# Kernel optimization log

Measured on AMD Instinct MI355X. Metric: run time of the kernel, lower is better.

The kernel has to match this reference:

```python
import jax, jax.numpy as jnp
import numpy as np

E1 = 150000   # number of 1-hop edges
E2 = 150000   # number of 2-hop edges
T = 400000    # triangles per triangle class
C = 64        # in_channels
H = 64        # mlp_hidden_channels
L = 2         # num DR2FWL2Conv layers
N_MLP = 8     # MLPs per conv layer


def setup_inputs() -> dict:
    key = jax.random.key(0)
    ks = jax.random.split(key, 20)
    edge_attr = jax.random.normal(ks[0], (E1, C), jnp.float32)
    edge_attr2 = jax.random.normal(ks[1], (E2, C), jnp.float32)
    # triangle index tensors: rows (ij, ik, kj); hop type of each row decides the range
    triangle_1_1_1 = jax.random.randint(ks[2], (3, T), 0, E1)
    triangle_1_1_2 = jnp.stack([jax.random.randint(jax.random.fold_in(ks[3], r), (T,), 0, m)
                                for r, m in enumerate([E1, E1, E2])])
    triangle_1_2_2 = jnp.stack([jax.random.randint(jax.random.fold_in(ks[4], r), (T,), 0, m)
                                for r, m in enumerate([E1, E2, E2])])
    triangle_2_2_2 = jax.random.randint(ks[5], (3, T), 0, E2)
    inverse_edge_1 = jax.random.permutation(ks[6], E1)
    inverse_edge_2 = jax.random.permutation(ks[7], E2)
    s = 0.05
    mlp_w1 = jax.random.normal(ks[8], (L, N_MLP, C, H), jnp.float32) * s
    mlp_b1 = jnp.zeros((L, N_MLP, H), jnp.float32)
    mlp_w2 = jax.random.normal(ks[9], (L, N_MLP, H, C), jnp.float32) * s
    mlp_b2 = jnp.zeros((L, N_MLP, C), jnp.float32)
    lin_w1 = jax.random.normal(ks[10], (C, C), jnp.float32) * s
    lin_b1 = jnp.zeros((C,), jnp.float32)
    lin_w2 = jax.random.normal(ks[11], (C, C), jnp.float32) * s
    lin_b2 = jnp.zeros((C,), jnp.float32)
    return dict(edge_attr=edge_attr, edge_attr2=edge_attr2,
                triangle_1_1_1=triangle_1_1_1, triangle_1_1_2=triangle_1_1_2,
                triangle_1_2_2=triangle_1_2_2, triangle_2_2_2=triangle_2_2_2,
                inverse_edge_1=inverse_edge_1, inverse_edge_2=inverse_edge_2,
                mlp_w1=mlp_w1, mlp_b1=mlp_b1, mlp_w2=mlp_w2, mlp_b2=mlp_b2,
                lin_w1=lin_w1, lin_b1=lin_b1, lin_w2=lin_w2, lin_b2=lin_b2)


def reference(edge_attr, edge_attr2, triangle_1_1_1, triangle_1_1_2,
              triangle_1_2_2, triangle_2_2_2, inverse_edge_1, inverse_edge_2,
              mlp_w1, mlp_b1, mlp_w2, mlp_b2, lin_w1, lin_b1, lin_w2, lin_b2):
    eps = 0.0
    eps2 = 0.0
    ij111, ik111, kj111 = triangle_1_1_1
    ij112, ik112, kj112 = triangle_1_1_2
    ij122, ik122, kj122 = triangle_1_2_2
    ij222, ik222, kj222 = triangle_2_2_2
    seg = jax.ops.segment_sum

    e1, e2 = edge_attr, edge_attr2
    n1, n2 = e1.shape[0], e2.shape[0]
    for li in range(mlp_w1.shape[0]):
        def mlp(x, mi, li=li):
            h = jax.nn.relu(x @ mlp_w1[li, mi] + mlp_b1[li, mi])
            return h @ mlp_w2[li, mi] + mlp_b2[li, mi]
        m111 = seg(mlp(e1[ik111], 0) * mlp(e1[kj111], 0), ij111, num_segments=n1)
        m112 = seg(mlp(e1[ik112], 1) * mlp(e2[kj112], 2), ij112, num_segments=n1)
        m122 = seg(mlp(e2[ik122], 3) * mlp(e2[kj122], 3), ij122, num_segments=n1)
        e1 = e1 * (1.0 + eps) + m111 + m112 + m112[inverse_edge_1] + m122
        m211 = seg(mlp(e1[ij112], 4) * mlp(e1[ik112], 4), kj112, num_segments=n2)
        m212 = seg(mlp(e1[ij122], 5) * mlp(e2[kj122], 6), ik122, num_segments=n2)
        m222 = seg(mlp(e2[ik222], 7) * mlp(e2[kj222], 7), ij222, num_segments=n2)
        e2 = e2 * (1.0 + eps2) + m211 + m212 + m212[inverse_edge_2] + m222
        # norm=None (Identity), relu after, dropout=0 in eval
        e1, e2 = jax.nn.relu(e1), jax.nn.relu(e2)
    return (e1 @ lin_w1 + lin_b1, e2 @ lin_w2 + lin_b2)
```

## Files before the change

kernel.cpp:

```cpp
#include <hip/hip_runtime.h>
#include <hip/hip_fp16.h>


typedef unsigned short u16;
typedef unsigned int u32;
typedef _Float16 f16;
typedef __attribute__((ext_vector_type(8))) short s16x8;
typedef __attribute__((ext_vector_type(4))) float f32x4;
typedef __attribute__((ext_vector_type(4))) _Float16 f16x4;

#define MFMA16(a, b, c) __builtin_amdgcn_mfma_f32_16x16x32_bf16((a), (b), (c), 0, 0, 0)

static __device__ __forceinline__ u16 bf16_rne(float x) {
  u32 u = __float_as_uint(x);
  return (u16)((u + 0x7fffu + ((u >> 16) & 1u)) >> 16);
}
static __device__ __forceinline__ float bf16_f32(u16 h) {
  return __uint_as_float(((u32)h) << 16);
}
static __device__ __forceinline__ void cvt_hilo8(const f32x4 a, const f32x4 b, s16x8& hi, s16x8& lo) {
#pragma unroll
  for (int j = 0; j < 4; j++) {
    float x = a[j];
    u16 h = bf16_rne(x);
    u16 l = bf16_rne(x - bf16_f32(h));
    hi[j] = (short)h; lo[j] = (short)l;
  }
#pragma unroll
  for (int j = 0; j < 4; j++) {
    float x = b[j];
    u16 h = bf16_rne(x);
    u16 l = bf16_rne(x - bf16_f32(h));
    hi[4 + j] = (short)h; lo[4 + j] = (short)l;
  }
}

__global__ __launch_bounds__(256) void repack_split_kernel(const float* __restrict__ src,
                                                           u16* __restrict__ hi, u16* __restrict__ lo, int nmat) {
  int o = blockIdx.x * 256 + threadIdx.x;
  int stride = gridDim.x * 256;
  int total = nmat * 4096;
  for (; o < total; o += stride) {
    int m = o >> 12, r = o & 4095;
    int j = r & 7, lane = (r >> 3) & 63, nt = (r >> 9) & 3, kt = (r >> 11) & 1;
    int k = kt * 32 + ((lane >> 4) << 3) + j;
    int n = nt * 16 + (lane & 15);
    float x = src[(size_t)m * 4096 + k * 64 + n];
    u16 h = bf16_rne(x);
    hi[o] = h;
    lo[o] = bf16_rne(x - bf16_f32(h));
  }
}

__global__ __launch_bounds__(256) void copy_kernel(const float* __restrict__ src, float* __restrict__ dst, int n4) {
  int i = blockIdx.x * 256 + threadIdx.x;
  int stride = gridDim.x * 256;
  const f32x4* s4 = (const f32x4*)src;
  f32x4* d4 = (f32x4*)dst;
  for (; i < n4; i += stride) d4[i] = s4[i];
}

__global__ __launch_bounds__(256) void relu_kernel(float* __restrict__ e, int n4) {
  int i = blockIdx.x * 256 + threadIdx.x;
  int stride = gridDim.x * 256;
  f32x4* e4 = (f32x4*)e;
  for (; i < n4; i += stride) {
    f32x4 v = e4[i];
#pragma unroll
    for (int j = 0; j < 4; j++) v[j] = fmaxf(v[j], 0.0f);
    e4[i] = v;
  }
}

template <bool DO_RELU>
__global__ __launch_bounds__(256) void addinv2_kernel(float* __restrict__ e, const f16* __restrict__ A,
                                                      const f16* __restrict__ B, const int* __restrict__ inv, int E) {
  int i = blockIdx.x * 256 + threadIdx.x;
  int stride = gridDim.x * 256;
  int total = E * 16;
  f32x4* e4 = (f32x4*)e;
  const f16x4* A4 = (const f16x4*)A;
  const f16x4* B4 = (const f16x4*)B;
  for (; i < total; i += stride) {
    int r = i >> 4, q = i & 15;
    int ir = inv[r];
    f32x4 v = e4[i];
    f16x4 a = A4[i];
    f16x4 b = B4[i];
    f16x4 bi = B4[(size_t)ir * 16 + q];
#pragma unroll
    for (int j = 0; j < 4; j++) {
      float x = v[j] + (float)a[j] + (float)b[j] + (float)bi[j];
      v[j] = DO_RELU ? fmaxf(x, 0.0f) : x;
    }
    e4[i] = v;
  }
}

__global__ __launch_bounds__(256) void seg3_kernel(
    __half2* __restrict__ dstA, __half2* __restrict__ dstB,
    const __half2* __restrict__ paA, const __half2* __restrict__ pbA,
    const int* __restrict__ iA0, const int* __restrict__ iA1, const int* __restrict__ iA2,
    const __half2* __restrict__ paB, const __half2* __restrict__ pbB,
    const int* __restrict__ iB0, const int* __restrict__ iB1, const int* __restrict__ iB2,
    const __half2* __restrict__ paC, const __half2* __restrict__ pbC,
    const int* __restrict__ iC0, const int* __restrict__ iC1, const int* __restrict__ iC2,
    int T) {
  int i = blockIdx.x * 256 + threadIdx.x;
  int stride = gridDim.x * 256;
  int total = 3 * T * 32;
  for (; i < total; i += stride) {
    int u = i >> 5, cp = i & 31;
    __half2* dst;
    const __half2 *pa, *pb;
    const int *i0, *i1, *i2;
    int t;
    if (u < T) { t = u; dst = dstA; pa = paA; pb = pbA; i0 = iA0; i1 = iA1; i2 = iA2; }
    else if (u < 2 * T) { t = u - T; dst = dstB; pa = paB; pb = pbB; i0 = iB0; i1 = iB1; i2 = iB2; }
    else { t = u - 2 * T; dst = dstA; pa = paC; pb = pbC; i0 = iC0; i1 = iC1; i2 = iC2; }
    __half2 va = pa[(size_t)i1[t] * 32 + cp];
    __half2 vb = pb[(size_t)i2[t] * 32 + cp];
    float2 fa = __half22float2(va), fb = __half22float2(vb);
    __half2 prod = __floats2half2_rn(fa.x * fb.x, fa.y * fb.y);
    unsafeAtomicAdd(&dst[(size_t)i0[t] * 32 + cp], prod);
  }
}

__global__ __launch_bounds__(256) void mlp4_kernel(
    const float* __restrict__ srcA, const float* __restrict__ srcB,
    f16* __restrict__ d0, f16* __restrict__ d1, f16* __restrict__ d2, f16* __restrict__ d3,
    const u16* __restrict__ w1h_, const u16* __restrict__ w1l_,
    const u16* __restrict__ w2h_, const u16* __restrict__ w2l_,
    const float* __restrict__ b1_, const float* __restrict__ b2_, int s1, int s2) {
  __shared__ float hshm[4][1024];
  const int tid = threadIdx.x;
  const int wave = tid >> 6, lane = tid & 63;
  const int lrow = lane & 15, lk = lane >> 4;
  const int gw = (blockIdx.x * 256 + tid) >> 6;
  const int total = 2 * s1 + 2 * s2;
  if (gw >= total) return;

  int mi, strip;
  const float* src;
  f16* dst;
  if (gw < s1) { mi = 0; strip = gw; src = srcA; dst = d0; }
  else if (gw < 2 * s1) { mi = 1; strip = gw - s1; src = srcA; dst = d1; }
  else if (gw < 2 * s1 + s2) { mi = 2; strip = gw - 2 * s1; src = srcB; dst = d2; }
  else { mi = 3; strip = gw - 2 * s1 - s2; src = srcB; dst = d3; }

  const s16x8* W1H = (const s16x8*)(w1h_ + (size_t)mi * 4096);
  const s16x8* W1L = (const s16x8*)(w1l_ + (size_t)mi * 4096);
  const s16x8* W2H = (const s16x8*)(w2h_ + (size_t)mi * 4096);
  const s16x8* W2L = (const s16x8*)(w2l_ + (size_t)mi * 4096);
  s16x8 w1h[2][4], w1l[2][4], w2h[2][4], w2l[2][4];
#pragma unroll
  for (int kt = 0; kt < 2; kt++)
#pragma unroll
    for (int nt = 0; nt < 4; nt++) {
      const int f = (kt * 4 + nt) * 64 + lane;
      w1h[kt][nt] = W1H[f];
      w1l[kt][nt] = W1L[f];
      w2h[kt][nt] = W2H[f];
      w2l[kt][nt] = W2L[f];
    }
  float bias1[4], bias2[4];
#pragma unroll
  for (int nt = 0; nt < 4; nt++) {
    bias1[nt] = b1_[mi * 64 + nt * 16 + lrow];
    bias2[nt] = b2_[mi * 64 + nt * 16 + lrow];
  }

  float* hl = hshm[wave];
  const float* xp = src + (size_t)(strip * 16 + lrow) * 64 + lk * 8;
  f32x4 x0 = *(const f32x4*)(xp + 0);
  f32x4 x1 = *(const f32x4*)(xp + 4);
  f32x4 x2 = *(const f32x4*)(xp + 32);
  f32x4 x3 = *(const f32x4*)(xp + 36);
  s16x8 ah[2], al[2];
  cvt_hilo8(x0, x1, ah[0], al[0]);
  cvt_hilo8(x2, x3, ah[1], al[1]);

  f32x4 acc[4];
#pragma unroll
  for (int nt = 0; nt < 4; nt++) { acc[nt][0] = bias1[nt]; acc[nt][1] = bias1[nt]; acc[nt][2] = bias1[nt]; acc[nt][3] = bias1[nt]; }
#pragma unroll
  for (int kt = 0; kt < 2; kt++)
#pragma unroll
    for (int nt = 0; nt < 4; nt++) {
      acc[nt] = MFMA16(ah[kt], w1h[kt][nt], acc[nt]);
      acc[nt] = MFMA16(ah[kt], w1l[kt][nt], acc[nt]);
      acc[nt] = MFMA16(al[kt], w1h[kt][nt], acc[nt]);
    }

#pragma unroll
  for (int nt = 0; nt < 4; nt++)
#pragma unroll
    for (int r = 0; r < 4; r++) {
      const int row = lk * 4 + r;
      const int col = nt * 16 + lrow;
      hl[row * 64 + (col ^ ((row & 7) << 2))] = fmaxf(acc[nt][r], 0.0f);
    }
  s16x8 bh[2], bl[2];
#pragma unroll
  for (int kt = 0; kt < 2; kt++) {
    const int colb = kt * 32 + lk * 8;
    const int xr = (lrow & 7) << 2;
    f32x4 h0 = *(const f32x4*)&hl[lrow * 64 + ((colb + 0) ^ xr)];
    f32x4 h1 = *(const f32x4*)&hl[lrow * 64 + ((colb + 4) ^ xr)];
    cvt_hilo8(h0, h1, bh[kt], bl[kt]);
  }

  f32x4 out[4];
#pragma unroll
  for (int nt = 0; nt < 4; nt++) { out[nt][0] = bias2[nt]; out[nt][1] = bias2[nt]; out[nt][2] = bias2[nt]; out[nt][3] = bias2[nt]; }
#pragma unroll
  for (int kt = 0; kt < 2; kt++)
#pragma unroll
    for (int nt = 0; nt < 4; nt++) {
      out[nt] = MFMA16(bh[kt], w2h[kt][nt], out[nt]);
      out[nt] = MFMA16(bh[kt], w2l[kt][nt], out[nt]);
      out[nt] = MFMA16(bl[kt], w2h[kt][nt], out[nt]);
    }

  f16* dp = dst + (size_t)strip * 1024;
#pragma unroll
  for (int nt = 0; nt < 4; nt++)
#pragma unroll
    for (int r = 0; r < 4; r++)
      dp[(lk * 4 + r) * 64 + nt * 16 + lrow] = (f16)out[nt][r];
}

__global__ __launch_bounds__(256) void lin_kernel(const float* __restrict__ src, float* __restrict__ dst,
                                                  const u16* __restrict__ wh_, const u16* __restrict__ wl_,
                                                  const float* __restrict__ b_, int nstrips) {
  const int tid = threadIdx.x;
  const int wave = tid >> 6, lane = tid & 63;
  const int lrow = lane & 15, lk = lane >> 4;

  const s16x8* WH = (const s16x8*)wh_;
  const s16x8* WL = (const s16x8*)wl_;
  s16x8 wh[2][4], wl[2][4];
#pragma unroll
  for (int kt = 0; kt < 2; kt++)
#pragma unroll
    for (int nt = 0; nt < 4; nt++) {
      const int f = (kt * 4 + nt) * 64 + lane;
      wh[kt][nt] = WH[f];
      wl[kt][nt] = WL[f];
    }
  float bias[4];
#pragma unroll
  for (int nt = 0; nt < 4; nt++) bias[nt] = b_[nt * 16 + lrow];

  for (int s = blockIdx.x * 4 + wave; s < nstrips; s += gridDim.x * 4) {
    const float* xp = src + (size_t)(s * 16 + lrow) * 64 + lk * 8;
    f32x4 x0 = *(const f32x4*)(xp + 0);
    f32x4 x1 = *(const f32x4*)(xp + 4);
    f32x4 x2 = *(const f32x4*)(xp + 32);
    f32x4 x3 = *(const f32x4*)(xp + 36);
    s16x8 ah[2], al[2];
    cvt_hilo8(x0, x1, ah[0], al[0]);
    cvt_hilo8(x2, x3, ah[1], al[1]);

    f32x4 acc[4];
#pragma unroll
    for (int nt = 0; nt < 4; nt++) { acc[nt][0] = bias[nt]; acc[nt][1] = bias[nt]; acc[nt][2] = bias[nt]; acc[nt][3] = bias[nt]; }
#pragma unroll
    for (int kt = 0; kt < 2; kt++)
#pragma unroll
      for (int nt = 0; nt < 4; nt++) {
        acc[nt] = MFMA16(ah[kt], wh[kt][nt], acc[nt]);
        acc[nt] = MFMA16(ah[kt], wl[kt][nt], acc[nt]);
        acc[nt] = MFMA16(al[kt], wh[kt][nt], acc[nt]);
      }
    float* dp = dst + (size_t)s * 1024;
#pragma unroll
    for (int nt = 0; nt < 4; nt++)
#pragma unroll
      for (int r = 0; r < 4; r++)
        dp[(lk * 4 + r) * 64 + nt * 16 + lrow] = acc[nt][r];
  }
}

extern "C" void kernel_launch(void* const* d_in, const int* in_sizes, int n_in,
                              void* d_out, int out_size, void* d_ws, size_t ws_size,
                              hipStream_t stream) {
  const float* in_e1 = (const float*)d_in[0];
  const float* in_e2 = (const float*)d_in[1];
  const int* t111 = (const int*)d_in[2];
  const int* t112 = (const int*)d_in[3];
  const int* t122 = (const int*)d_in[4];
  const int* t222 = (const int*)d_in[5];
  const int* inv1 = (const int*)d_in[6];
  const int* inv2 = (const int*)d_in[7];
  const float* mw1 = (const float*)d_in[8];
  const float* mb1 = (const float*)d_in[9];
  const float* mw2 = (const float*)d_in[10];
  const float* mb2 = (const float*)d_in[11];
  const float* lw1 = (const float*)d_in[12];
  const float* lb1 = (const float*)d_in[13];
  const float* lw2 = (const float*)d_in[14];
  const float* lb2 = (const float*)d_in[15];

  const int E1 = in_sizes[0] / 64, E2 = in_sizes[1] / 64;
  const int T = in_sizes[2] / 3;
  const int L = in_sizes[8] / (8 * 64 * 64);
  const size_t nE1 = (size_t)E1 * 64, nE2 = (size_t)E2 * 64;
  const size_t nMax = nE1 > nE2 ? nE1 : nE2;

  float* e1b = (float*)d_ws;
  float* e2b = e1b + nE1;
  f16* mA = (f16*)(e2b + nE2);
  f16* mB = mA + nMax;
  f16* p0 = mB + nMax;
  f16* p1 = p0 + nE1;
  const size_t wmat = (size_t)L * 8 * 4096;
  u16* w1h = (u16*)(p1 + nE1);
  u16* w1l = w1h + wmat;
  u16* w2h = w1l + wmat;
  u16* w2l = w2h + wmat;
  u16* lwh = w2l + wmat;
  u16* lwl = lwh + 8192;
  const size_t needB = (nE1 + nE2) * 4 + (2 * nMax + 2 * nE1) * 2 + (4 * wmat + 4 * 4096) * 2;
  if (ws_size < needB) return;

  f16* p2 = (f16*)d_out;
  f16* p3 = p2 + nE2;

  const int s1 = E1 / 16, s2 = E2 / 16;
  const int mlp4B = (2 * s1 + 2 * s2 + 3) / 4;
  const int SEGB = 2048, ELTB = 2048;

  repack_split_kernel<<<256, 256, 0, stream>>>(mw1, w1h, w1l, L * 8);
  repack_split_kernel<<<256, 256, 0, stream>>>(mw2, w2h, w2l, L * 8);
  repack_split_kernel<<<32, 256, 0, stream>>>(lw1, lwh, lwl, 1);
  repack_split_kernel<<<32, 256, 0, stream>>>(lw2, lwh + 4096, lwl + 4096, 1);

  copy_kernel<<<ELTB, 256, 0, stream>>>(in_e1, e1b, (int)(nE1 / 4));
  copy_kernel<<<ELTB, 256, 0, stream>>>(in_e2, e2b, (int)(nE2 / 4));

  for (int li = 0; li < L; li++) {
    const size_t mo = (size_t)li * 8 * 4096;
    const size_t bo = (size_t)li * 8 * 64;
    mlp4_kernel<<<mlp4B, 256, 0, stream>>>(e1b, e2b, p0, p1, p2, p3,
                                           w1h + mo, w1l + mo, w2h + mo, w2l + mo,
                                           mb1 + bo, mb2 + bo, s1, s2);
    hipMemsetAsync(mA, 0, 2 * nMax * 2, stream);
    seg3_kernel<<<SEGB, 256, 0, stream>>>(
        (__half2*)mA, (__half2*)mB,
        (const __half2*)p0, (const __half2*)p0, t111, t111 + T, t111 + 2 * T,
        (const __half2*)p1, (const __half2*)p2, t112, t112 + T, t112 + 2 * T,
        (const __half2*)p3, (const __half2*)p3, t122, t122 + T, t122 + 2 * T, T);
    addinv2_kernel<false><<<ELTB, 256, 0, stream>>>(e1b, mA, mB, inv1, E1);

    mlp4_kernel<<<mlp4B, 256, 0, stream>>>(e1b, e2b, p0, p1, p2, p3,
                                           w1h + mo + 4 * 4096, w1l + mo + 4 * 4096,
                                           w2h + mo + 4 * 4096, w2l + mo + 4 * 4096,
                                           mb1 + bo + 4 * 64, mb2 + bo + 4 * 64, s1, s2);
    hipMemsetAsync(mA, 0, 2 * nMax * 2, stream);
    seg3_kernel<<<SEGB, 256, 0, stream>>>(
        (__half2*)mA, (__half2*)mB,
        (const __half2*)p0, (const __half2*)p0, t112 + 2 * T, t112, t112 + T,
        (const __half2*)p1, (const __half2*)p2, t122 + T, t122, t122 + 2 * T,
        (const __half2*)p3, (const __half2*)p3, t222, t222 + T, t222 + 2 * T, T);
    addinv2_kernel<true><<<ELTB, 256, 0, stream>>>(e2b, mA, mB, inv2, E2);

    relu_kernel<<<ELTB, 256, 0, stream>>>(e1b, (int)(nE1 / 4));
  }

  lin_kernel<<<(s1 + 3) / 4, 256, 0, stream>>>(e1b, (float*)d_out, lwh, lwl, lb1, s1);
  lin_kernel<<<(s2 + 3) / 4, 256, 0, stream>>>(e2b, (float*)d_out + nE1, lwh + 4096, lwl + 4096, lb2, s2);
}
```

Before: 992.0 us.

## Replace atomic segment-sum scatter with CSR gather built once by counting sort

Builds per-class CSR row pointers and (A,B) index payloads once per call via histogram, three-pass scan, and scatter. Each segment-sum then becomes a gather kernel where one thread owns an output row/channel pair, accumulates in fp32 and adds straight into the edge features. This removes the fp16 atomic adds, the memsets and one accumulator buffer. The cost is a preprocessing pass with atomics on every call and uneven per-row loop lengths in the gather.

```diff
diff --git a/kernel.cpp b/kernel.cpp
--- a/kernel.cpp
+++ b/kernel.cpp
@@ -7,7 +7,6 @@
 typedef _Float16 f16;
 typedef __attribute__((ext_vector_type(8))) short s16x8;
 typedef __attribute__((ext_vector_type(4))) float f32x4;
-typedef __attribute__((ext_vector_type(4))) _Float16 f16x4;
 
 #define MFMA16(a, b, c) __builtin_amdgcn_mfma_f32_16x16x32_bf16((a), (b), (c), 0, 0, 0)
 
@@ -33,6 +32,140 @@
     u16 l = bf16_rne(x - bf16_f32(h));
     hi[4 + j] = (short)h; lo[4 + j] = (short)l;
   }
+}
+
+static __device__ __forceinline__ void class_ptrs(int c, const int* t111, const int* t112,
+                                                  const int* t122, const int* t222, int T,
+                                                  const int*& D, const int*& A, const int*& B) {
+  switch (c) {
+    case 0: D = t111;          A = t111 + T; B = t111 + 2 * T; break;
+    case 1: D = t112;          A = t112 + T; B = t112 + 2 * T; break;
+    case 2: D = t122;          A = t122 + T; B = t122 + 2 * T; break;
+    case 3: D = t112 + 2 * T;  A = t112;     B = t112 + T;     break;
+    case 4: D = t122 + T;      A = t122;     B = t122 + 2 * T; break;
+    default: D = t222;         A = t222 + T; B = t222 + 2 * T; break;
+  }
+}
+
+__global__ __launch_bounds__(256) void hist_kernel(int* __restrict__ pos,
+                                                   const int* t111, const int* t112,
+                                                   const int* t122, const int* t222, int T, int Emax) {
+  int i = blockIdx.x * 256 + threadIdx.x;
+  if (i >= 6 * T) return;
+  int c = i / T, t = i - c * T;
+  const int *D, *A, *B;
+  class_ptrs(c, t111, t112, t122, t222, T, D, A, B);
+  atomicAdd(&pos[(size_t)c * Emax + D[t]], 1);
+}
+
+__global__ __launch_bounds__(1024) void scanA_kernel(const int* __restrict__ pos, int* __restrict__ partial,
+                                                     int Emax, int E1, int E2, int NCH) {
+  __shared__ int sh[1024];
+  int c = blockIdx.x / NCH, ch = blockIdx.x % NCH;
+  int idx = ch * 1024 + threadIdx.x;
+  int Ec = c < 3 ? E1 : E2;
+  int v = (idx < Ec) ? pos[(size_t)c * Emax + idx] : 0;
+  sh[threadIdx.x] = v;
+  __syncthreads();
+  for (int s = 512; s > 0; s >>= 1) {
+    if (threadIdx.x < s) sh[threadIdx.x] += sh[threadIdx.x + s];
+    __syncthreads();
+  }
+  if (threadIdx.x == 0) partial[blockIdx.x] = sh[0];
+}
+
+__global__ __launch_bounds__(1024) void scanB_kernel(int* __restrict__ partial, int NCH) {
+  __shared__ int sh[1024];
+  for (int c = 0; c < 6; c++) {
+    int v = (threadIdx.x < NCH) ? partial[c * NCH + threadIdx.x] : 0;
+    sh[threadIdx.x] = v;
+    __syncthreads();
+    for (int off = 1; off < 1024; off <<= 1) {
+      int x = (threadIdx.x >= off) ? sh[threadIdx.x - off] : 0;
+      __syncthreads();
+      sh[threadIdx.x] += x;
+      __syncthreads();
+    }
+    if (threadIdx.x < NCH) partial[c * NCH + threadIdx.x] = sh[threadIdx.x] - v;
+    __syncthreads();
+  }
+}
+
+__global__ __launch_bounds__(1024) void scanC_kernel(int* __restrict__ pos, int* __restrict__ rp,
+                                                     const int* __restrict__ partial,
+                                                     int Emax, int E1, int E2, int NCH, int T) {
+  __shared__ int sh[1024];
+  int c = blockIdx.x / NCH, ch = blockIdx.x % NCH;
+  int idx = ch * 1024 + threadIdx.x;
+  int Ec = c < 3 ? E1 : E2;
+  int v = (idx < Ec) ? pos[(size_t)c * Emax + idx] : 0;
+  sh[threadIdx.x] = v;
+  __syncthreads();
+  for (int off = 1; off < 1024; off <<= 1) {
+    int x = (threadIdx.x >= off) ? sh[threadIdx.x - off] : 0;
+    __syncthreads();
+    sh[threadIdx.x] += x;
+    __syncthreads();
+  }
+  int excl = sh[threadIdx.x] - v;
+  int base = partial[blockIdx.x];
+  if (idx < Ec) {
+    int off = base + excl;
+    rp[(size_t)c * (Emax + 1) + idx] = off;
+    pos[(size_t)c * Emax + idx] = off;
+    if (idx == Ec - 1) rp[(size_t)c * (Emax + 1) + Ec] = off + v;
+  }
+}
+
+typedef struct { int x, y; } i2;
+
+__global__ __launch_bounds__(256) void scatter_kernel(int* __restrict__ pos, i2* __restrict__ payload,
+                                                      const int* t111, const int* t112,
+                                                      const int* t122, const int* t222, int T, int Emax) {
+  int i = blockIdx.x * 256 + threadIdx.x;
+  if (i >= 6 * T) return;
+  int c = i / T, t = i - c * T;
+  const int *D, *A, *B;
+  class_ptrs(c, t111, t112, t122, t222, T, D, A, B);
+  int slot = atomicAdd(&pos[(size_t)c * Emax + D[t]], 1);
+  i2 p; p.x = A[t]; p.y = B[t];
+  payload[(size_t)c * T + slot] = p;
+}
+
+__global__ __launch_bounds__(256) void segcsr_kernel(
+    float2* __restrict__ e, float2* __restrict__ mB,
+    const int* __restrict__ rpA, const i2* __restrict__ plA, const __half2* __restrict__ paA, const __half2* __restrict__ pbA,
+    const int* __restrict__ rpB, const i2* __restrict__ plB, const __half2* __restrict__ paB, const __half2* __restrict__ pbB,
+    const int* __restrict__ rpC, const i2* __restrict__ plC, const __half2* __restrict__ paC, const __half2* __restrict__ pbC,
+    int E) {
+  int i = blockIdx.x * 256 + threadIdx.x;
+  if (i >= E * 32) return;
+  int r = i >> 5, cp = i & 31;
+  float2 acc = e[(size_t)r * 32 + cp];
+  int b0 = rpA[r], b1 = rpA[r + 1];
+  for (int t = b0; t < b1; t++) {
+    i2 ab = plA[t];
+    float2 a = __half22float2(paA[(size_t)ab.x * 32 + cp]);
+    float2 b = __half22float2(pbA[(size_t)ab.y * 32 + cp]);
+    acc.x += a.x * b.x; acc.y += a.y * b.y;
+  }
+  b0 = rpC[r]; b1 = rpC[r + 1];
+  for (int t = b0; t < b1; t++) {
+    i2 ab = plC[t];
+    float2 a = __half22float2(paC[(size_t)ab.x * 32 + cp]);
+    float2 b = __half22float2(pbC[(size_t)ab.y * 32 + cp]);
+    acc.x += a.x * b.x; acc.y += a.y * b.y;
+  }
+  e[(size_t)r * 32 + cp] = acc;
+  float2 accB = make_float2(0.0f, 0.0f);
+  b0 = rpB[r]; b1 = rpB[r + 1];
+  for (int t = b0; t < b1; t++) {
+    i2 ab = plB[t];
+    float2 a = __half22float2(paB[(size_t)ab.x * 32 + cp]);
+    float2 b = __half22float2(pbB[(size_t)ab.y * 32 + cp]);
+    accB.x += a.x * b.x; accB.y += a.y * b.y;
+  }
+  mB[(size_t)r * 32 + cp] = accB;
 }
 
 __global__ __launch_bounds__(256) void repack_split_kernel(const float* __restrict__ src,
@@ -73,56 +206,25 @@
 }
 
 template <bool DO_RELU>
-__global__ __launch_bounds__(256) void addinv2_kernel(float* __restrict__ e, const f16* __restrict__ A,
-                                                      const f16* __restrict__ B, const int* __restrict__ inv, int E) {
+__global__ __launch_bounds__(256) void addinv_kernel(float* __restrict__ e, const float* __restrict__ B,
+                                                     const int* __restrict__ inv, int E) {
   int i = blockIdx.x * 256 + threadIdx.x;
   int stride = gridDim.x * 256;
   int total = E * 16;
   f32x4* e4 = (f32x4*)e;
-  const f16x4* A4 = (const f16x4*)A;
-  const f16x4* B4 = (const f16x4*)B;
+  const f32x4* B4 = (const f32x4*)B;
   for (; i < total; i += stride) {
     int r = i >> 4, q = i & 15;
     int ir = inv[r];
     f32x4 v = e4[i];
-    f16x4 a = A4[i];
-    f16x4 b = B4[i];
-    f16x4 bi = B4[(size_t)ir * 16 + q];
+    f32x4 b = B4[i];
+    f32x4 bi = B4[(size_t)ir * 16 + q];
 #pragma unroll
     for (int j = 0; j < 4; j++) {
-      float x = v[j] + (float)a[j] + (float)b[j] + (float)bi[j];
+      float x = v[j] + b[j] + bi[j];
       v[j] = DO_RELU ? fmaxf(x, 0.0f) : x;
     }
     e4[i] = v;
-  }
-}
-
-__global__ __launch_bounds__(256) void seg3_kernel(
-    __half2* __restrict__ dstA, __half2* __restrict__ dstB,
-    const __half2* __restrict__ paA, const __half2* __restrict__ pbA,
-    const int* __restrict__ iA0, const int* __restrict__ iA1, const int* __restrict__ iA2,
-    const __half2* __restrict__ paB, const __half2* __restrict__ pbB,
-    const int* __restrict__ iB0, const int* __restrict__ iB1, const int* __restrict__ iB2,
-    const __half2* __restrict__ paC, const __half2* __restrict__ pbC,
-    const int* __restrict__ iC0, const int* __restrict__ iC1, const int* __restrict__ iC2,
-    int T) {
-  int i = blockIdx.x * 256 + threadIdx.x;
-  int stride = gridDim.x * 256;
-  int total = 3 * T * 32;
-  for (; i < total; i += stride) {
-    int u = i >> 5, cp = i & 31;
-    __half2* dst;
-    const __half2 *pa, *pb;
-    const int *i0, *i1, *i2;
-    int t;
-    if (u < T) { t = u; dst = dstA; pa = paA; pb = pbA; i0 = iA0; i1 = iA1; i2 = iA2; }
-    else if (u < 2 * T) { t = u - T; dst = dstB; pa = paB; pb = pbB; i0 = iB0; i1 = iB1; i2 = iB2; }
-    else { t = u - 2 * T; dst = dstA; pa = paC; pb = pbC; i0 = iC0; i1 = iC1; i2 = iC2; }
-    __half2 va = pa[(size_t)i1[t] * 32 + cp];
-    __half2 vb = pb[(size_t)i2[t] * 32 + cp];
-    float2 fa = __half22float2(va), fb = __half22float2(vb);
-    __half2 prod = __floats2half2_rn(fa.x * fb.x, fa.y * fb.y);
-    unsafeAtomicAdd(&dst[(size_t)i0[t] * 32 + cp], prod);
   }
 }
 
@@ -305,14 +407,16 @@
   const int E1 = in_sizes[0] / 64, E2 = in_sizes[1] / 64;
   const int T = in_sizes[2] / 3;
   const int L = in_sizes[8] / (8 * 64 * 64);
+  const int Emax = E1 > E2 ? E1 : E2;
   const size_t nE1 = (size_t)E1 * 64, nE2 = (size_t)E2 * 64;
-  const size_t nMax = nE1 > nE2 ? nE1 : nE2;
+  const size_t nMax = (size_t)Emax * 64;
+  const int NCH = (Emax + 1023) / 1024;
 
   float* e1b = (float*)d_ws;
   float* e2b = e1b + nE1;
-  f16* mA = (f16*)(e2b + nE2);
-  f16* mB = mA + nMax;
-  f16* p0 = mB + nMax;
+  float* mB = e2b + nE2;
+  i2* payload = (i2*)(mB + nMax);
+  f16* p0 = (f16*)(payload + (size_t)6 * T);
   f16* p1 = p0 + nE1;
   const size_t wmat = (size_t)L * 8 * 4096;
   u16* w1h = (u16*)(p1 + nE1);
@@ -321,7 +425,10 @@
   u16* w2l = w2h + wmat;
   u16* lwh = w2l + wmat;
   u16* lwl = lwh + 8192;
-  const size_t needB = (nE1 + nE2) * 4 + (2 * nMax + 2 * nE1) * 2 + (4 * wmat + 4 * 4096) * 2;
+  int* rp = (int*)(lwl + 8192);
+  int* pos = rp + (size_t)6 * (Emax + 1);
+  int* partial = pos + (size_t)6 * Emax;
+  const size_t needB = (char*)(partial + (size_t)6 * NCH) - (char*)d_ws + 64;
   if (ws_size < needB) return;
 
   f16* p2 = (f16*)d_out;
@@ -329,41 +436,48 @@
 
   const int s1 = E1 / 16, s2 = E2 / 16;
   const int mlp4B = (2 * s1 + 2 * s2 + 3) / 4;
-  const int SEGB = 2048, ELTB = 2048;
+  const int ELTB = 2048;
+  const int histB = (6 * T + 255) / 256;
+  const int segB1 = (E1 * 32 + 255) / 256, segB2 = (E2 * 32 + 255) / 256;
+
+  hipMemsetAsync(pos, 0, (size_t)6 * Emax * 4, stream);
+  hist_kernel<<<histB, 256, 0, stream>>>(pos, t111, t112, t122, t222, T, Emax);
+  scanA_kernel<<<6 * NCH, 1024, 0, stream>>>(pos, partial, Emax, E1, E2, NCH);
+  scanB_kernel<<<1, 1024, 0, stream>>>(partial, NCH);
+  scanC_kernel<<<6 * NCH, 1024, 0, stream>>>(pos, rp, partial, Emax, E1, E2, NCH, T);
+  scatter_kernel<<<histB, 256, 0, stream>>>(pos, payload, t111, t112, t122, t222, T, Emax);
 
   repack_split_kernel<<<256, 256, 0, stream>>>(mw1, w1h, w1l, L * 8);
   repack_split_kernel<<<256, 256, 0, stream>>>(mw2, w2h, w2l, L * 8);
   repack_split_kernel<<<32, 256, 0, stream>>>(lw1, lwh, lwl, 1);
   repack_split_kernel<<<32, 256, 0, stream>>>(lw2, lwh + 4096, lwl + 4096, 1);
-
   copy_kernel<<<ELTB, 256, 0, stream>>>(in_e1, e1b, (int)(nE1 / 4));
   copy_kernel<<<ELTB, 256, 0, stream>>>(in_e2, e2b, (int)(nE2 / 4));
 
+  const int EP1 = Emax + 1;
   for (int li = 0; li < L; li++) {
     const size_t mo = (size_t)li * 8 * 4096;
     const size_t bo = (size_t)li * 8 * 64;
     mlp4_kernel<<<mlp4B, 256, 0, stream>>>(e1b, e2b, p0, p1, p2, p3,
                                            w1h + mo, w1l + mo, w2h + mo, w2l + mo,
                                            mb1 + bo, mb2 + bo, s1, s2);
-    hipMemsetAsync(mA, 0, 2 * nMax * 2, stream);
-    seg3_kernel<<<SEGB, 256, 0, stream>>>(
-        (__half2*)mA, (__half2*)mB,
-        (const __half2*)p0, (const __half2*)p0, t111, t111 + T, t111 + 2 * T,
-        (const __half2*)p1, (const __half2*)p2, t112, t112 + T, t112 + 2 * T,
-        (const __half2*)p3, (const __half2*)p3, t122, t122 + T, t122 + 2 * T, T);
-    addinv2_kernel<false><<<ELTB, 256, 0, stream>>>(e1b, mA, mB, inv1, E1);
+    segcsr_kernel<<<segB1, 256, 0, stream>>>(
+        (float2*)e1b, (float2*)mB,
+        rp + 0 * EP1, payload + (size_t)0 * T, (const __half2*)p0, (const __half2*)p0,
+        rp + 1 * EP1, payload + (size_t)1 * T, (const __half2*)p1, (const __half2*)p2,
+        rp + 2 * EP1, payload + (size_t)2 * T, (const __half2*)p3, (const __half2*)p3, E1);
+    addinv_kernel<false><<<ELTB, 256, 0, stream>>>(e1b, mB, inv1, E1);
 
     mlp4_kernel<<<mlp4B, 256, 0, stream>>>(e1b, e2b, p0, p1, p2, p3,
                                            w1h + mo + 4 * 4096, w1l + mo + 4 * 4096,
                                            w2h + mo + 4 * 4096, w2l + mo + 4 * 4096,
                                            mb1 + bo + 4 * 64, mb2 + bo + 4 * 64, s1, s2);
-    hipMemsetAsync(mA, 0, 2 * nMax * 2, stream);
-    seg3_kernel<<<SEGB, 256, 0, stream>>>(
-        (__half2*)mA, (__half2*)mB,
-        (const __half2*)p0, (const __half2*)p0, t112 + 2 * T, t112, t112 + T,
-        (const __half2*)p1, (const __half2*)p2, t122 + T, t122, t122 + 2 * T,
-        (const __half2*)p3, (const __half2*)p3, t222, t222 + T, t222 + 2 * T, T);
-    addinv2_kernel<true><<<ELTB, 256, 0, stream>>>(e2b, mA, mB, inv2, E2);
+    segcsr_kernel<<<segB2, 256, 0, stream>>>(
+        (float2*)e2b, (float2*)mB,
+        rp + 3 * EP1, payload + (size_t)3 * T, (const __half2*)p0, (const __half2*)p0,
+        rp + 4 * EP1, payload + (size_t)4 * T, (const __half2*)p1, (const __half2*)p2,
+        rp + 5 * EP1, payload + (size_t)5 * T, (const __half2*)p3, (const __half2*)p3, E2);
+    addinv_kernel<true><<<ELTB, 256, 0, stream>>>(e2b, mB, inv2, E2);
 
     relu_kernel<<<ELTB, 256, 0, stream>>>(e1b, (int)(nE1 / 4));
   }
```

Result: slower. 1.151 ms (+16.0%).

## Persistent grouped MLP launches, rebalance MLP stages, fuse final ReLU into linear

Applied to the files above, without the earlier changes.

The per-layer MLP kernel becomes a persistent, grid-strided kernel in which each block handles one MLP unit. It loads that unit's weights into registers once and reuses them across many 16-row strips, instead of reloading them for every strip. The MLPs on e2 (6, 7) do not depend on the updated e1, so they move into the first launch, leaving only MLPs 4 and 5 for the second launch. The last layer's e1 ReLU is folded into the final linear kernel, which removes one elementwise pass. In exchange, the kernel needs more output buffers (held in d_out) and a fixed grid of 256 blocks per unit, which may balance work poorly across units.

```diff
diff --git a/kernel.cpp b/kernel.cpp
--- a/kernel.cpp
+++ b/kernel.cpp
@@ -126,27 +126,26 @@
   }
 }
 
-__global__ __launch_bounds__(256) void mlp4_kernel(
-    const float* __restrict__ srcA, const float* __restrict__ srcB,
-    f16* __restrict__ d0, f16* __restrict__ d1, f16* __restrict__ d2, f16* __restrict__ d3,
+__global__ __launch_bounds__(256) void mlpN_kernel(
+    const float* __restrict__ e1s, const float* __restrict__ e2s,
+    f16* __restrict__ d0, f16* __restrict__ d1, f16* __restrict__ d2,
+    f16* __restrict__ d3, f16* __restrict__ d4, f16* __restrict__ d5,
     const u16* __restrict__ w1h_, const u16* __restrict__ w1l_,
     const u16* __restrict__ w2h_, const u16* __restrict__ w2l_,
-    const float* __restrict__ b1_, const float* __restrict__ b2_, int s1, int s2) {
+    const float* __restrict__ b1_, const float* __restrict__ b2_,
+    int miPacked, int selMask, int nUnits, int s1, int s2, int BPU) {
   __shared__ float hshm[4][1024];
+  const int u = blockIdx.x / BPU;
+  if (u >= nUnits) return;
   const int tid = threadIdx.x;
   const int wave = tid >> 6, lane = tid & 63;
   const int lrow = lane & 15, lk = lane >> 4;
-  const int gw = (blockIdx.x * 256 + tid) >> 6;
-  const int total = 2 * s1 + 2 * s2;
-  if (gw >= total) return;
-
-  int mi, strip;
-  const float* src;
-  f16* dst;
-  if (gw < s1) { mi = 0; strip = gw; src = srcA; dst = d0; }
-  else if (gw < 2 * s1) { mi = 1; strip = gw - s1; src = srcA; dst = d1; }
-  else if (gw < 2 * s1 + s2) { mi = 2; strip = gw - 2 * s1; src = srcB; dst = d2; }
-  else { mi = 3; strip = gw - 2 * s1 - s2; src = srcB; dst = d3; }
+
+  const int mi = (miPacked >> (4 * u)) & 15;
+  const int sel = (selMask >> u) & 1;
+  const float* src = sel ? e2s : e1s;
+  const int strips = sel ? s2 : s1;
+  f16* dst = (u == 0) ? d0 : (u == 1) ? d1 : (u == 2) ? d2 : (u == 3) ? d3 : (u == 4) ? d4 : d5;
 
   const s16x8* W1H = (const s16x8*)(w1h_ + (size_t)mi * 4096);
   const s16x8* W1L = (const s16x8*)(w1l_ + (size_t)mi * 4096);
@@ -171,65 +170,69 @@
   }
 
   float* hl = hshm[wave];
-  const float* xp = src + (size_t)(strip * 16 + lrow) * 64 + lk * 8;
-  f32x4 x0 = *(const f32x4*)(xp + 0);
-  f32x4 x1 = *(const f32x4*)(xp + 4);
-  f32x4 x2 = *(const f32x4*)(xp + 32);
-  f32x4 x3 = *(const f32x4*)(xp + 36);
-  s16x8 ah[2], al[2];
-  cvt_hilo8(x0, x1, ah[0], al[0]);
-  cvt_hilo8(x2, x3, ah[1], al[1]);
-
-  f32x4 acc[4];
-#pragma unroll
-  for (int nt = 0; nt < 4; nt++) { acc[nt][0] = bias1[nt]; acc[nt][1] = bias1[nt]; acc[nt][2] = bias1[nt]; acc[nt][3] = bias1[nt]; }
-#pragma unroll
-  for (int kt = 0; kt < 2; kt++)
-#pragma unroll
-    for (int nt = 0; nt < 4; nt++) {
-      acc[nt] = MFMA16(ah[kt], w1h[kt][nt], acc[nt]);
-      acc[nt] = MFMA16(ah[kt], w1l[kt][nt], acc[nt]);
-      acc[nt] = MFMA16(al[kt], w1h[kt][nt], acc[nt]);
-    }
-
-#pragma unroll
-  for (int nt = 0; nt < 4; nt++)
-#pragma unroll
-    for (int r = 0; r < 4; r++) {
-      const int row = lk * 4 + r;
-      const int col = nt * 16 + lrow;
-      hl[row * 64 + (col ^ ((row & 7) << 2))] = fmaxf(acc[nt][r], 0.0f);
-    }
-  s16x8 bh[2], bl[2];
-#pragma unroll
-  for (int kt = 0; kt < 2; kt++) {
-    const int colb = kt * 32 + lk * 8;
-    const int xr = (lrow & 7) << 2;
-    f32x4 h0 = *(const f32x4*)&hl[lrow * 64 + ((colb + 0) ^ xr)];
-    f32x4 h1 = *(const f32x4*)&hl[lrow * 64 + ((colb + 4) ^ xr)];
-    cvt_hilo8(h0, h1, bh[kt], bl[kt]);
-  }
-
-  f32x4 out[4];
-#pragma unroll
-  for (int nt = 0; nt < 4; nt++) { out[nt][0] = bias2[nt]; out[nt][1] = bias2[nt]; out[nt][2] = bias2[nt]; out[nt][3] = bias2[nt]; }
-#pragma unroll
-  for (int kt = 0; kt < 2; kt++)
-#pragma unroll
-    for (int nt = 0; nt < 4; nt++) {
-      out[nt] = MFMA16(bh[kt], w2h[kt][nt], out[nt]);
-      out[nt] = MFMA16(bh[kt], w2l[kt][nt], out[nt]);
-      out[nt] = MFMA16(bl[kt], w2h[kt][nt], out[nt]);
-    }
-
-  f16* dp = dst + (size_t)strip * 1024;
-#pragma unroll
-  for (int nt = 0; nt < 4; nt++)
-#pragma unroll
-    for (int r = 0; r < 4; r++)
-      dp[(lk * 4 + r) * 64 + nt * 16 + lrow] = (f16)out[nt][r];
-}
-
+  const int lb = blockIdx.x % BPU;
+  for (int strip = lb * 4 + wave; strip < strips; strip += BPU * 4) {
+    const float* xp = src + (size_t)(strip * 16 + lrow) * 64 + lk * 8;
+    f32x4 x0 = *(const f32x4*)(xp + 0);
+    f32x4 x1 = *(const f32x4*)(xp + 4);
+    f32x4 x2 = *(const f32x4*)(xp + 32);
+    f32x4 x3 = *(const f32x4*)(xp + 36);
+    s16x8 ah[2], al[2];
+    cvt_hilo8(x0, x1, ah[0], al[0]);
+    cvt_hilo8(x2, x3, ah[1], al[1]);
+
+    f32x4 acc[4];
+#pragma unroll
+    for (int nt = 0; nt < 4; nt++) { acc[nt][0] = bias1[nt]; acc[nt][1] = bias1[nt]; acc[nt][2] = bias1[nt]; acc[nt][3] = bias1[nt]; }
+#pragma unroll
+    for (int kt = 0; kt < 2; kt++)
+#pragma unroll
+      for (int nt = 0; nt < 4; nt++) {
+        acc[nt] = MFMA16(ah[kt], w1h[kt][nt], acc[nt]);
+        acc[nt] = MFMA16(ah[kt], w1l[kt][nt], acc[nt]);
+        acc[nt] = MFMA16(al[kt], w1h[kt][nt], acc[nt]);
+      }
+
+#pragma unroll
+    for (int nt = 0; nt < 4; nt++)
+#pragma unroll
+      for (int r = 0; r < 4; r++) {
+        const int row = lk * 4 + r;
+        const int col = nt * 16 + lrow;
+        hl[row * 64 + (col ^ ((row & 7) << 2))] = fmaxf(acc[nt][r], 0.0f);
+      }
+    s16x8 bh[2], bl[2];
+#pragma unroll
+    for (int kt = 0; kt < 2; kt++) {
+      const int colb = kt * 32 + lk * 8;
+      const int xr = (lrow & 7) << 2;
+      f32x4 h0 = *(const f32x4*)&hl[lrow * 64 + ((colb + 0) ^ xr)];
+      f32x4 h1 = *(const f32x4*)&hl[lrow * 64 + ((colb + 4) ^ xr)];
+      cvt_hilo8(h0, h1, bh[kt], bl[kt]);
+    }
+
+    f32x4 out[4];
+#pragma unroll
+    for (int nt = 0; nt < 4; nt++) { out[nt][0] = bias2[nt]; out[nt][1] = bias2[nt]; out[nt][2] = bias2[nt]; out[nt][3] = bias2[nt]; }
+#pragma unroll
+    for (int kt = 0; kt < 2; kt++)
+#pragma unroll
+      for (int nt = 0; nt < 4; nt++) {
+        out[nt] = MFMA16(bh[kt], w2h[kt][nt], out[nt]);
+        out[nt] = MFMA16(bh[kt], w2l[kt][nt], out[nt]);
+        out[nt] = MFMA16(bl[kt], w2h[kt][nt], out[nt]);
+      }
+
+    f16* dp = dst + (size_t)strip * 1024;
+#pragma unroll
+    for (int nt = 0; nt < 4; nt++)
+#pragma unroll
+      for (int r = 0; r < 4; r++)
+        dp[(lk * 4 + r) * 64 + nt * 16 + lrow] = (f16)out[nt][r];
+  }
+}
+
+template <bool RELU>
 __global__ __launch_bounds__(256) void lin_kernel(const float* __restrict__ src, float* __restrict__ dst,
                                                   const u16* __restrict__ wh_, const u16* __restrict__ wl_,
                                                   const float* __restrict__ b_, int nstrips) {
@@ -258,6 +261,13 @@
     f32x4 x1 = *(const f32x4*)(xp + 4);
     f32x4 x2 = *(const f32x4*)(xp + 32);
     f32x4 x3 = *(const f32x4*)(xp + 36);
+    if (RELU) {
+#pragma unroll
+      for (int j = 0; j < 4; j++) {
+        x0[j] = fmaxf(x0[j], 0.0f); x1[j] = fmaxf(x1[j], 0.0f);
+        x2[j] = fmaxf(x2[j], 0.0f); x3[j] = fmaxf(x3[j], 0.0f);
+      }
+    }
     s16x8 ah[2], al[2];
     cvt_hilo8(x0, x1, ah[0], al[0]);
     cvt_hilo8(x2, x3, ah[1], al[1]);
@@ -312,62 +322,68 @@
   float* e2b = e1b + nE1;
   f16* mA = (f16*)(e2b + nE2);
   f16* mB = mA + nMax;
-  f16* p0 = mB + nMax;
-  f16* p1 = p0 + nE1;
+  f16* q0 = mB + nMax;
+  f16* q1 = q0 + nE1;
   const size_t wmat = (size_t)L * 8 * 4096;
-  u16* w1h = (u16*)(p1 + nE1);
+  u16* w1h = (u16*)(q1 + nE1);
   u16* w1l = w1h + wmat;
   u16* w2h = w1l + wmat;
   u16* w2l = w2h + wmat;
   u16* lwh = w2l + wmat;
   u16* lwl = lwh + 8192;
-  const size_t needB = (nE1 + nE2) * 4 + (2 * nMax + 2 * nE1) * 2 + (4 * wmat + 4 * 4096) * 2;
+  const size_t needB = (nE1 + nE2) * 4 + (2 * nMax + 2 * nE1) * 2 + (4 * wmat + 4 * 4096) * 2 + 64;
   if (ws_size < needB) return;
 
-  f16* p2 = (f16*)d_out;
-  f16* p3 = p2 + nE2;
+  f16* q2 = (f16*)d_out;
+  f16* q3 = q2 + nE2;
+  f16* q6 = q3 + nE2;
+  f16* q7 = q6 + nE2;
+  f16* q4 = q0;
+  f16* q5 = q1;
 
   const int s1 = E1 / 16, s2 = E2 / 16;
-  const int mlp4B = (2 * s1 + 2 * s2 + 3) / 4;
-  const int SEGB = 2048, ELTB = 2048;
+  const int SEGB = 2048, ELTB = 2048, BPU = 256, LINB = 256;
 
   repack_split_kernel<<<256, 256, 0, stream>>>(mw1, w1h, w1l, L * 8);
   repack_split_kernel<<<256, 256, 0, stream>>>(mw2, w2h, w2l, L * 8);
   repack_split_kernel<<<32, 256, 0, stream>>>(lw1, lwh, lwl, 1);
   repack_split_kernel<<<32, 256, 0, stream>>>(lw2, lwh + 4096, lwl + 4096, 1);
-
   copy_kernel<<<ELTB, 256, 0, stream>>>(in_e1, e1b, (int)(nE1 / 4));
   copy_kernel<<<ELTB, 256, 0, stream>>>(in_e2, e2b, (int)(nE2 / 4));
 
   for (int li = 0; li < L; li++) {
-    const size_t mo = (size_t)li * 8 * 4096;
-    const size_t bo = (size_t)li * 8 * 64;
-    mlp4_kernel<<<mlp4B, 256, 0, stream>>>(e1b, e2b, p0, p1, p2, p3,
-                                           w1h + mo, w1l + mo, w2h + mo, w2l + mo,
-                                           mb1 + bo, mb2 + bo, s1, s2);
+    const u16* W1H = w1h + (size_t)li * 8 * 4096;
+    const u16* W1L = w1l + (size_t)li * 8 * 4096;
+    const u16* W2H = w2h + (size_t)li * 8 * 4096;
+    const u16* W2L = w2l + (size_t)li * 8 * 4096;
+    const float* B1 = mb1 + (size_t)li * 8 * 64;
+    const float* B2 = mb2 + (size_t)li * 8 * 64;
+
+    mlpN_kernel<<<6 * BPU, 256, 0, stream>>>(e1b, e2b, q0, q1, q2, q3, q6, q7,
+                                             W1H, W1L, W2H, W2L, B1, B2,
+                                             0x763210, 0x3C, 6, s1, s2, BPU);
     hipMemsetAsync(mA, 0, 2 * nMax * 2, stream);
     seg3_kernel<<<SEGB, 256, 0, stream>>>(
         (__half2*)mA, (__half2*)mB,
-        (const __half2*)p0, (const __half2*)p0, t111, t111 + T, t111 + 2 * T,
-        (const __half2*)p1, (const __half2*)p2, t112, t112 + T, t112 + 2 * T,
-        (const __half2*)p3, (const __half2*)p3, t122, t122 + T, t122 + 2 * T, T);
+        (const __half2*)q0, (const __half2*)q0, t111, t111 + T, t111 + 2 * T,
+        (const __half2*)q1, (const __half2*)q2, t112, t112 + T, t112 + 2 * T,
+        (const __half2*)q3, (const __half2*)q3, t122, t122 + T, t122 + 2 * T, T);
     addinv2_kernel<false><<<ELTB, 256, 0, stream>>>(e1b, mA, mB, inv1, E1);
 
-    mlp4_kernel<<<mlp4B, 256, 0, stream>>>(e1b, e2b, p0, p1, p2, p3,
-                                           w1h + mo + 4 * 4096, w1l + mo + 4 * 4096,
-                                           w2h + mo + 4 * 4096, w2l + mo + 4 * 4096,
-                                           mb1 + bo + 4 * 64, mb2 + bo + 4 * 64, s1, s2);
+    mlpN_kernel<<<2 * BPU, 256, 0, stream>>>(e1b, e2b, q4, q5, q2, q3, q6, q7,
+                                             W1H, W1L, W2H, W2L, B1, B2,
+                                             0x54, 0x0, 2, s1, s2, BPU);
+    if (li < L - 1) relu_kernel<<<ELTB, 256, 0, stream>>>(e1b, (int)(nE1 / 4));
+
     hipMemsetAsync(mA, 0, 2 * nMax * 2, stream);
     seg3_kernel<<<SEGB, 256, 0, stream>>>(
         (__half2*)mA, (__half2*)mB,
-        (const __half2*)p0, (const __half2*)p0, t112 + 2 * T, t112, t112 + T,
-        (const __half2*)p1, (const __half2*)p2, t122 + T, t122, t122 + 2 * T,
-        (const __half2*)p3, (const __half2*)p3, t222, t222 + T, t222 + 2 * T, T);
+        (const __half2*)q4, (const __half2*)q4, t112 + 2 * T, t112, t112 + T,
+        (const __half2*)q5, (const __half2*)q6, t122 + T, t122, t122 + 2 * T,
+        (const __half2*)q7, (const __half2*)q7, t222, t222 + T, t222 + 2 * T, T);
     addinv2_kernel<true><<<ELTB, 256, 0, stream>>>(e2b, mA, mB, inv2, E2);
-
-    relu_kernel<<<ELTB, 256, 0, stream>>>(e1b, (int)(nE1 / 4));
-  }
-
-  lin_kernel<<<(s1 + 3) / 4, 256, 0, stream>>>(e1b, (float*)d_out, lwh, lwl, lb1, s1);
-  lin_kernel<<<(s2 + 3) / 4, 256, 0, stream>>>(e2b, (float*)d_out + nE1, lwh + 4096, lwl + 4096, lb2, s2);
-}
+  }
+
+  lin_kernel<true><<<LINB, 256, 0, stream>>>(e1b, (float*)d_out, lwh, lwl, lb1, s1);
+  lin_kernel<false><<<LINB, 256, 0, stream>>>(e2b, (float*)d_out + nE1, lwh + 4096, lwl + 4096, lb2, s2);
+}
```

Result: faster. 896.1 us (-9.7%).
